# Kernel optimization log

Measured on AMD Instinct MI355X. Metric: run time of the kernel, lower is better.

Reference implementation:

```python
import jax, jax.numpy as jnp
import numpy as np

B, S, D = 4, 4096, 2048
L = 3  # conv kernel size (L_cache)


def setup_inputs() -> dict:
    key = jax.random.key(0)
    k1, k2, k3, k4 = jax.random.split(key, 4)
    scale_in = 1.0 / np.sqrt(D)
    return {
        "x": jax.random.normal(k1, (B, S, D), dtype=jnp.float32),
        "W_in": jax.random.normal(k2, (D, 3 * D), dtype=jnp.float32) * scale_in,
        "conv_w": jax.random.normal(k3, (D, L), dtype=jnp.float32) * (1.0 / np.sqrt(L)),
        "W_out": jax.random.normal(k4, (D, D), dtype=jnp.float32) * scale_in,
    }


def _causal_depthwise_conv(bx, conv_w):
    # bx: [B, D, S], conv_w: [D, L]; causal cross-correlation per channel
    rhs = conv_w[:, None, :]  # [D, 1, L] = (out_ch, in_ch/groups, width)
    return jax.lax.conv_general_dilated(
        bx, rhs,
        window_strides=(1,),
        padding=[(L - 1, 0)],
        dimension_numbers=("NCH", "OIH", "NCH"),
        feature_group_count=bx.shape[1],
    )


def reference(x, W_in, conv_w, W_out):
    # in_proj: [B,S,D] @ [D,3D] -> [B,S,3D]
    BCx = jnp.einsum("bsd,de->bse", x, W_in)
    B_gate, C_gate, x_proj = jnp.split(BCx, 3, axis=-1)  # each [B,S,D]
    Bx = (B_gate * x_proj).transpose(0, 2, 1)            # [B,D,S]
    conv_out = _causal_depthwise_conv(Bx, conv_w)         # [B,D,S]
    y = C_gate * conv_out.transpose(0, 2, 1)              # [B,S,D]
    return jnp.einsum("bsd,de->bse", y, W_out)            # [B,S,D]
```

## Files before the change

kernel.cpp:

```cpp
#include <hip/hip_runtime.h>
#include <cstddef>
#include <cstdint>

#define D_DIM 2048
#define S_DIM 4096
#define B_DIM 4
#define M_DIM (B_DIM * S_DIM)
#define N1_DIM (3 * D_DIM)

typedef short bf16x8 __attribute__((ext_vector_type(8)));
typedef float f32x4  __attribute__((ext_vector_type(4)));

typedef const unsigned int __attribute__((address_space(1))) gu32_t;
typedef unsigned int       __attribute__((address_space(3))) lu32_t;

__device__ __forceinline__ unsigned short f2bf(float f) {
    unsigned int u = __float_as_uint(f);
    u += 0x7FFFu + ((u >> 16) & 1u);
    return (unsigned short)(u >> 16);
}
__device__ __forceinline__ float bf2f(unsigned short h) {
    return __uint_as_float(((unsigned int)h) << 16);
}

__global__ void k_convert(const float* __restrict__ in, unsigned short* __restrict__ out, int n8) {
    int i = blockIdx.x * blockDim.x + threadIdx.x;
    if (i >= n8) return;
    const float4* p = (const float4*)in + (size_t)i * 2;
    float4 a = p[0];
    float4 b = p[1];
    union { unsigned short s[8]; uint4 v; } r;
    r.s[0] = f2bf(a.x); r.s[1] = f2bf(a.y); r.s[2] = f2bf(a.z); r.s[3] = f2bf(a.w);
    r.s[4] = f2bf(b.x); r.s[5] = f2bf(b.y); r.s[6] = f2bf(b.z); r.s[7] = f2bf(b.w);
    ((uint4*)out)[i] = r.v;
}

__global__ void k_transpose(const float* __restrict__ in, unsigned short* __restrict__ out,
                            int R, int C) {
    __shared__ float t[32][33];
    int c0 = blockIdx.x * 32, r0 = blockIdx.y * 32;
    int x = threadIdx.x;
    for (int yy = threadIdx.y; yy < 32; yy += 8)
        t[yy][x] = in[(size_t)(r0 + yy) * C + c0 + x];
    __syncthreads();
    for (int yy = threadIdx.y; yy < 32; yy += 8)
        out[(size_t)(c0 + yy) * R + r0 + x] = f2bf(t[x][yy]);
}

template <bool OUT_BF16>
__global__ __launch_bounds__(256, 2)
void k_gemm(const unsigned short* __restrict__ A, const unsigned short* __restrict__ Bt,
            void* __restrict__ Cp, int N, int K) {
    __shared__ unsigned short As[128 * 64];
    __shared__ unsigned short Bs[128 * 64];

    const int tid  = threadIdx.x;
    const int wave = tid >> 6;
    const int lane = tid & 63;
    const int m0 = blockIdx.y * 128;
    const int n0 = blockIdx.x * 128;
    const int wm = (wave & 1) * 64;
    const int wn = (wave >> 1) * 64;

    f32x4 acc[4][4] = {};

    const int srow = lane >> 3;
    const int gd   = lane & 7;
    const int quad = lane >> 4;
    const int rsel = lane & 15;

    const int KT = K >> 6;
    for (int kt = 0; kt < KT; ++kt) {
        const int k0 = kt << 6;
        __syncthreads();
        #pragma unroll
        for (int i = 0; i < 4; ++i) {
            const int seg = i * 4 + wave;
            const int row = seg * 8 + srow;
            const int gs  = gd ^ (row & 7);
            const unsigned short* ga = A  + (size_t)(m0 + row) * K + k0 + gs * 8;
            const unsigned short* gb = Bt + (size_t)(n0 + row) * K + k0 + gs * 8;
            __builtin_amdgcn_global_load_lds((gu32_t*)ga, (lu32_t*)(As + seg * 512), 16, 0, 0);
            __builtin_amdgcn_global_load_lds((gu32_t*)gb, (lu32_t*)(Bs + seg * 512), 16, 0, 0);
        }
        __syncthreads();

        #pragma unroll
        for (int kb = 0; kb < 2; ++kb) {
            bf16x8 af[4], bfr[4];
            #pragma unroll
            for (int i = 0; i < 4; ++i) {
                const int ra = wm + i * 16 + rsel;
                const int ga = (kb * 4 + quad) ^ (ra & 7);
                af[i] = *(const bf16x8*)&As[ra * 64 + ga * 8];
                const int rb = wn + i * 16 + rsel;
                const int gb = (kb * 4 + quad) ^ (rb & 7);
                bfr[i] = *(const bf16x8*)&Bs[rb * 64 + gb * 8];
            }
            #pragma unroll
            for (int i = 0; i < 4; ++i)
                #pragma unroll
                for (int j = 0; j < 4; ++j)
                    acc[i][j] = __builtin_amdgcn_mfma_f32_16x16x32_bf16(af[i], bfr[j], acc[i][j], 0, 0, 0);
        }
    }

    #pragma unroll
    for (int i = 0; i < 4; ++i) {
        #pragma unroll
        for (int j = 0; j < 4; ++j) {
            const int col  = n0 + wn + j * 16 + rsel;
            const int rowb = m0 + wm + i * 16 + quad * 4;
            #pragma unroll
            for (int r = 0; r < 4; ++r) {
                const size_t off = (size_t)(rowb + r) * N + col;
                if (OUT_BF16) ((unsigned short*)Cp)[off] = f2bf(acc[i][j][r]);
                else          ((float*)Cp)[off] = acc[i][j][r];
            }
        }
    }
}

__global__ void k_conv_gate(const unsigned short* __restrict__ BCx,
                            const float* __restrict__ conv_w,
                            unsigned short* __restrict__ y) {
    const int bs = blockIdx.x;
    const int s  = bs & (S_DIM - 1);
    const int d0 = threadIdx.x * 8;
    const size_t row = (size_t)bs * N1_DIM;

    union U8 { uint4 v; unsigned short s[8]; };
    float bx_m2[8], bx_m1[8], bx_0[8];
    #pragma unroll
    for (int j = 0; j < 8; ++j) { bx_m2[j] = 0.f; bx_m1[j] = 0.f; }

    U8 g, xp;
    g.v  = *(const uint4*)&BCx[row + d0];
    xp.v = *(const uint4*)&BCx[row + 2 * D_DIM + d0];
    #pragma unroll
    for (int j = 0; j < 8; ++j) bx_0[j] = bf2f(g.s[j]) * bf2f(xp.s[j]);

    if (s >= 1) {
        g.v  = *(const uint4*)&BCx[row - N1_DIM + d0];
        xp.v = *(const uint4*)&BCx[row - N1_DIM + 2 * D_DIM + d0];
        #pragma unroll
        for (int j = 0; j < 8; ++j) bx_m1[j] = bf2f(g.s[j]) * bf2f(xp.s[j]);
    }
    if (s >= 2) {
        g.v  = *(const uint4*)&BCx[row - 2 * N1_DIM + d0];
        xp.v = *(const uint4*)&BCx[row - 2 * N1_DIM + 2 * D_DIM + d0];
        #pragma unroll
        for (int j = 0; j < 8; ++j) bx_m2[j] = bf2f(g.s[j]) * bf2f(xp.s[j]);
    }

    U8 c; c.v = *(const uint4*)&BCx[row + D_DIM + d0];
    U8 r;
    #pragma unroll
    for (int j = 0; j < 8; ++j) {
        const float* w = conv_w + (size_t)(d0 + j) * 3;
        const float conv = w[0] * bx_m2[j] + w[1] * bx_m1[j] + w[2] * bx_0[j];
        r.s[j] = f2bf(bf2f(c.s[j]) * conv);
    }
    *(uint4*)&y[(size_t)bs * D_DIM + d0] = r.v;
}

extern "C" void kernel_launch(void* const* d_in, const int* in_sizes, int n_in,
                              void* d_out, int out_size, void* d_ws, size_t ws_size,
                              hipStream_t stream) {
    const float* x      = (const float*)d_in[0];
    const float* W_in   = (const float*)d_in[1];
    const float* conv_w = (const float*)d_in[2];
    const float* W_out  = (const float*)d_in[3];
    float* out = (float*)d_out;

    char* ws = (char*)d_ws;
    unsigned short* xb     = (unsigned short*)ws;
    unsigned short* Wt_in  = (unsigned short*)(ws + (size_t)67108864);
    unsigned short* Wt_out = (unsigned short*)(ws + (size_t)67108864 + 25165824);
    unsigned short* BCx    = (unsigned short*)(ws + (size_t)67108864 + 25165824 + 8388608);

    const int n8 = M_DIM * D_DIM / 8;
    k_convert<<<dim3((n8 + 255) / 256), 256, 0, stream>>>(x, xb, n8);
    k_transpose<<<dim3(N1_DIM / 32, D_DIM / 32), dim3(32, 8), 0, stream>>>(W_in, Wt_in, D_DIM, N1_DIM);
    k_transpose<<<dim3(D_DIM / 32, D_DIM / 32), dim3(32, 8), 0, stream>>>(W_out, Wt_out, D_DIM, D_DIM);

    k_gemm<true><<<dim3(N1_DIM / 128, M_DIM / 128), 256, 0, stream>>>(xb, Wt_in, BCx, N1_DIM, D_DIM);
    k_conv_gate<<<dim3(M_DIM), 256, 0, stream>>>(BCx, conv_w, xb );
    k_gemm<false><<<dim3(D_DIM / 128, M_DIM / 128), 256, 0, stream>>>(xb, Wt_out, out, D_DIM, D_DIM);
}
```

Measured before the change: 876.5 us.

## Replace GEMM with 256x256 double-buffered pipelined kernel and XCD-aware tile swizzle

Replaces the 128x128 single-buffer GEMM with a 256x256 tile kernel using 512 threads, double-buffered LDS and global-to-LDS loads interleaved across eight compute phases with fine-grained vmcnt waits and barriers. It adds MFMA priority raising and a block-index swizzle that groups consecutive tiles onto the same XCD for L2 reuse. The goal is to hide global load latency and raise arithmetic intensity per block. The cost is 128 KB of LDS per block plus heavy register use, which limits occupancy, and the hand-counted waitcnt scheduling is fragile.

```diff
diff --git a/kernel.cpp b/kernel.cpp
--- a/kernel.cpp
+++ b/kernel.cpp
@@ -47,75 +47,135 @@
         out[(size_t)(c0 + yy) * R + r0 + x] = f2bf(t[x][yy]);
 }
 
+__device__ __forceinline__ void stage_half(const unsigned short* __restrict__ src,
+                                           unsigned short* lds_base,
+                                           int rowbase, int half, int k0, int K, int tid) {
+    const int wave = tid >> 6;
+    #pragma unroll
+    for (int l = 0; l < 2; ++l) {
+        const int gidx = l * 512 + tid;
+        const int row  = gidx >> 3;
+        const int gs   = (gidx & 7) ^ (row & 7);
+        const unsigned short* g = src + (size_t)(rowbase + half * 128 + row) * K + k0 + gs * 8;
+        __builtin_amdgcn_global_load_lds((gu32_t*)g,
+            (lu32_t*)(lds_base + half * 8192 + (l * 512 + wave * 64) * 8), 16, 0, 0);
+    }
+}
+
 template <bool OUT_BF16>
-__global__ __launch_bounds__(256, 2)
-void k_gemm(const unsigned short* __restrict__ A, const unsigned short* __restrict__ Bt,
-            void* __restrict__ Cp, int N, int K) {
-    __shared__ unsigned short As[128 * 64];
-    __shared__ unsigned short Bs[128 * 64];
+__global__ __launch_bounds__(512, 2)
+void k_gemm256(const unsigned short* __restrict__ A, const unsigned short* __restrict__ Bt,
+               void* __restrict__ Cp, int N, int K) {
+    __shared__ unsigned short As[2][16384];
+    __shared__ unsigned short Bs[2][16384];
 
     const int tid  = threadIdx.x;
     const int wave = tid >> 6;
     const int lane = tid & 63;
-    const int m0 = blockIdx.y * 128;
-    const int n0 = blockIdx.x * 128;
-    const int wm = (wave & 1) * 64;
-    const int wn = (wave >> 1) * 64;
-
-    f32x4 acc[4][4] = {};
-
-    const int srow = lane >> 3;
-    const int gd   = lane & 7;
+    const int wm   = wave >> 2;
+    const int wn   = wave & 3;
     const int quad = lane >> 4;
     const int rsel = lane & 15;
+    (void)wave;
+
+    const int nbx  = gridDim.x;
+    const int nwg  = nbx * gridDim.y;
+    const int cpx  = nwg >> 3;
+    const int orig = blockIdx.y * nbx + blockIdx.x;
+    const int swz  = (orig & 7) * cpx + (orig >> 3);
+    const int m0 = (swz / nbx) * 256;
+    const int n0 = (swz % nbx) * 256;
+
+    f32x4 acc[8][4] = {};
 
     const int KT = K >> 6;
-    for (int kt = 0; kt < KT; ++kt) {
-        const int k0 = kt << 6;
-        __syncthreads();
-        #pragma unroll
-        for (int i = 0; i < 4; ++i) {
-            const int seg = i * 4 + wave;
-            const int row = seg * 8 + srow;
-            const int gs  = gd ^ (row & 7);
-            const unsigned short* ga = A  + (size_t)(m0 + row) * K + k0 + gs * 8;
-            const unsigned short* gb = Bt + (size_t)(n0 + row) * K + k0 + gs * 8;
-            __builtin_amdgcn_global_load_lds((gu32_t*)ga, (lu32_t*)(As + seg * 512), 16, 0, 0);
-            __builtin_amdgcn_global_load_lds((gu32_t*)gb, (lu32_t*)(Bs + seg * 512), 16, 0, 0);
+    const int NI = KT >> 1;
+
+    stage_half(A,  &As[0][0], m0, 0, 0,  K, tid);
+    stage_half(A,  &As[0][0], m0, 1, 0,  K, tid);
+    stage_half(Bt, &Bs[0][0], n0, 0, 0,  K, tid);
+    stage_half(Bt, &Bs[0][0], n0, 1, 0,  K, tid);
+    stage_half(Bt, &Bs[1][0], n0, 0, 64, K, tid);
+    stage_half(Bt, &Bs[1][0], n0, 1, 64, K, tid);
+    asm volatile("s_waitcnt vmcnt(4)" ::: "memory");
+    __builtin_amdgcn_s_barrier();
+
+    for (int i = 0; i < NI; ++i) {
+        const int kA  = i << 7;
+        const bool nxt = (i + 1 < NI);
+        #pragma unroll
+        for (int tt = 0; tt < 2; ++tt) {
+            const unsigned short* Asl = &As[tt][0];
+            const unsigned short* Bsl = &Bs[tt][0];
+            bf16x8 bfr[4][2];
+            #pragma unroll
+            for (int q = 0; q < 4; ++q) {
+                bf16x8 af[2][2];
+                #pragma unroll
+                for (int mi = 0; mi < 2; ++mi) {
+                    const int ra = wm * 128 + (q * 2 + mi) * 16 + rsel;
+                    #pragma unroll
+                    for (int kb = 0; kb < 2; ++kb) {
+                        const int g = (kb * 4 + quad) ^ (ra & 7);
+                        af[mi][kb] = *(const bf16x8*)&Asl[ra * 64 + g * 8];
+                    }
+                }
+                if (q == 0) {
+                    #pragma unroll
+                    for (int j = 0; j < 4; ++j) {
+                        const int rb = wn * 64 + j * 16 + rsel;
+                        #pragma unroll
+                        for (int kb = 0; kb < 2; ++kb) {
+                            const int g = (kb * 4 + quad) ^ (rb & 7);
+                            bfr[j][kb] = *(const bf16x8*)&Bsl[rb * 64 + g * 8];
+                        }
+                    }
+                }
+                const int ph = tt * 4 + q;
+                switch (ph) {
+                    case 0: stage_half(A,  &As[1][0], m0, 0, kA + 64,  K, tid); break;
+                    case 1: stage_half(A,  &As[1][0], m0, 1, kA + 64,  K, tid); break;
+                    case 2: if (nxt) stage_half(Bt, &Bs[0][0], n0, 0, kA + 128, K, tid); break;
+                    case 3: if (nxt) stage_half(Bt, &Bs[0][0], n0, 1, kA + 128, K, tid); break;
+                    case 4: if (nxt) stage_half(A,  &As[0][0], m0, 0, kA + 128, K, tid); break;
+                    case 5: if (nxt) stage_half(A,  &As[0][0], m0, 1, kA + 128, K, tid); break;
+                    case 6: if (nxt) stage_half(Bt, &Bs[1][0], n0, 0, kA + 192, K, tid); break;
+                    case 7: if (nxt) stage_half(Bt, &Bs[1][0], n0, 1, kA + 192, K, tid); break;
+                }
+                __builtin_amdgcn_s_barrier();
+                asm volatile("s_waitcnt lgkmcnt(0)" ::: "memory");
+                __builtin_amdgcn_s_setprio(1);
+                #pragma unroll
+                for (int kb = 0; kb < 2; ++kb)
+                    #pragma unroll
+                    for (int mi = 0; mi < 2; ++mi)
+                        #pragma unroll
+                        for (int j = 0; j < 4; ++j)
+                            acc[q * 2 + mi][j] = __builtin_amdgcn_mfma_f32_16x16x32_bf16(
+                                af[mi][kb], bfr[j][kb], acc[q * 2 + mi][j], 0, 0, 0);
+                __builtin_amdgcn_s_setprio(0);
+                if (ph == 3) {
+                    if (nxt) asm volatile("s_waitcnt vmcnt(4)" ::: "memory");
+                    else     asm volatile("s_waitcnt vmcnt(0)" ::: "memory");
+                } else if (ph == 7) {
+                    asm volatile("s_waitcnt vmcnt(4)" ::: "memory");
+                }
+                __builtin_amdgcn_s_barrier();
+            }
         }
-        __syncthreads();
-
-        #pragma unroll
-        for (int kb = 0; kb < 2; ++kb) {
-            bf16x8 af[4], bfr[4];
-            #pragma unroll
-            for (int i = 0; i < 4; ++i) {
-                const int ra = wm + i * 16 + rsel;
-                const int ga = (kb * 4 + quad) ^ (ra & 7);
-                af[i] = *(const bf16x8*)&As[ra * 64 + ga * 8];
-                const int rb = wn + i * 16 + rsel;
-                const int gb = (kb * 4 + quad) ^ (rb & 7);
-                bfr[i] = *(const bf16x8*)&Bs[rb * 64 + gb * 8];
-            }
-            #pragma unroll
-            for (int i = 0; i < 4; ++i)
-                #pragma unroll
-                for (int j = 0; j < 4; ++j)
-                    acc[i][j] = __builtin_amdgcn_mfma_f32_16x16x32_bf16(af[i], bfr[j], acc[i][j], 0, 0, 0);
-        }
-    }
-
-    #pragma unroll
-    for (int i = 0; i < 4; ++i) {
+    }
+
+    #pragma unroll
+    for (int fm = 0; fm < 8; ++fm) {
         #pragma unroll
         for (int j = 0; j < 4; ++j) {
-            const int col  = n0 + wn + j * 16 + rsel;
-            const int rowb = m0 + wm + i * 16 + quad * 4;
+            const int col  = n0 + wn * 64 + j * 16 + rsel;
+            const int rowb = m0 + wm * 128 + fm * 16 + quad * 4;
             #pragma unroll
             for (int r = 0; r < 4; ++r) {
                 const size_t off = (size_t)(rowb + r) * N + col;
-                if (OUT_BF16) ((unsigned short*)Cp)[off] = f2bf(acc[i][j][r]);
-                else          ((float*)Cp)[off] = acc[i][j][r];
+                if (OUT_BF16) ((unsigned short*)Cp)[off] = f2bf(acc[fm][j][r]);
+                else          ((float*)Cp)[off] = acc[fm][j][r];
             }
         }
     }
@@ -184,7 +244,7 @@
     k_transpose<<<dim3(N1_DIM / 32, D_DIM / 32), dim3(32, 8), 0, stream>>>(W_in, Wt_in, D_DIM, N1_DIM);
     k_transpose<<<dim3(D_DIM / 32, D_DIM / 32), dim3(32, 8), 0, stream>>>(W_out, Wt_out, D_DIM, D_DIM);
 
-    k_gemm<true><<<dim3(N1_DIM / 128, M_DIM / 128), 256, 0, stream>>>(xb, Wt_in, BCx, N1_DIM, D_DIM);
+    k_gemm256<true><<<dim3(N1_DIM / 256, M_DIM / 256), 512, 0, stream>>>(xb, Wt_in, BCx, N1_DIM, D_DIM);
     k_conv_gate<<<dim3(M_DIM), 256, 0, stream>>>(BCx, conv_w, xb );
-    k_gemm<false><<<dim3(D_DIM / 128, M_DIM / 128), 256, 0, stream>>>(xb, Wt_out, out, D_DIM, D_DIM);
-}
+    k_gemm256<false><<<dim3(D_DIM / 256, M_DIM / 256), 512, 0, stream>>>(xb, Wt_out, out, D_DIM, D_DIM);
+}
```

Result: no change. 873.9 us (-0.3%).
